# Optimization experiments

Hardware: AMD Instinct MI355X
Metric: run time of the kernel (lower is better)

## Reference

```python
import jax, jax.numpy as jnp
import numpy as np

NUM_HEADS = 16
KEY_DIM = 64
VALUE_DIM = 64
D_MODEL = 1024
NEG_INF = -1e10


def setup_inputs() -> dict:
    key = jax.random.key(0)
    ks = jax.random.split(key, 8)
    B, T, S, D = 4, 2048, 2048, D_MODEL
    w_scale = 1.0 / np.sqrt(D)  # keep logits well-scaled
    inp = {
        'query': jax.random.normal(ks[0], (B, T, D), jnp.float32),
        'key':   jax.random.normal(ks[1], (B, S, D), jnp.float32),
        'value': jax.random.normal(ks[2], (B, S, D), jnp.float32),
        'Wq': jax.random.normal(ks[3], (D, NUM_HEADS * KEY_DIM), jnp.float32) * w_scale,
        'bq': jnp.zeros((NUM_HEADS * KEY_DIM,), jnp.float32),
        'Wk': jax.random.normal(ks[4], (D, NUM_HEADS * KEY_DIM), jnp.float32) * w_scale,
        'bk': jnp.zeros((NUM_HEADS * KEY_DIM,), jnp.float32),
        'Wv': jax.random.normal(ks[5], (D, NUM_HEADS * VALUE_DIM), jnp.float32) * w_scale,
        'bv': jnp.zeros((NUM_HEADS * VALUE_DIM,), jnp.float32),
        'Wo': jax.random.normal(ks[6], (NUM_HEADS * VALUE_DIM, D), jnp.float32) * w_scale,
        'bo': jnp.zeros((D,), jnp.float32),
    }
    return inp


def reference(query, key, value, Wq, bq, Wk, bk, Wv, bv, Wo, bo):
    B, T, _ = query.shape
    S = key.shape[1]
    H, Dk, Dv = NUM_HEADS, KEY_DIM, VALUE_DIM
    # QKV projections -> (B, T/S, H, D_head)
    q = (query @ Wq + bq).reshape(B, T, H, Dk)
    k = (key @ Wk + bk).reshape(B, S, H, Dk)
    v = (value @ Wv + bv).reshape(B, S, H, Dv)
    # scaled dot-product scores: (B, H, T, S)
    q = q * (1.0 / jnp.sqrt(jnp.asarray(Dk, q.dtype)))
    scores = jnp.einsum('bthd,bshd->bhts', q, k)
    # causal mask [1,1,T,S], additive -1e10 on masked positions (as in source)
    causal = jnp.tril(jnp.ones((T, S), scores.dtype))
    scores = scores + NEG_INF * (1.0 - causal)
    attn = jax.nn.softmax(scores, axis=-1)
    # dropout rate = 0.0 -> identity
    ctx = jnp.einsum('bhts,bshd->bthd', attn, v).reshape(B, T, H * Dv)
    out = ctx @ Wo + bo
    return out
```

## Files before the change

kernel.cpp:

```cpp
#include <hip/hip_runtime.h>
#include <cstdint>

#define DEV static __device__ __forceinline__

typedef unsigned short u16;
typedef unsigned int u32;
using short8 = __attribute__((ext_vector_type(8))) short;
using f32x2  = __attribute__((ext_vector_type(2))) float;
using f32x4  = __attribute__((ext_vector_type(4))) float;
using f32x8  = __attribute__((ext_vector_type(8))) float;
using f32x16 = __attribute__((ext_vector_type(16))) float;
using u32x4  = __attribute__((ext_vector_type(4))) unsigned int;

constexpr int Bz = 4, Tz = 2048, Dz = 1024, Hz = 16;
constexpr float QSCALE = 0.125f * 1.4426950408889634f;

DEV u16 f2bf(float x) {
  union { float f; u32 u; } c; c.f = x;
  u32 u = c.u;
  return (u16)((u + 0x7FFFu + ((u >> 16) & 1u)) >> 16);
}

DEV u32 cvtpk(float a, float b) {
  u32 r;
  asm("v_cvt_pk_bf16_f32 %0, %1, %2" : "=v"(r) : "v"(a), "v"(b));
  return r;
}

DEV void gload16(const void* g, void* l) {
  __builtin_amdgcn_global_load_lds(
      (const __attribute__((address_space(1))) void*)g,
      (__attribute__((address_space(3))) void*)l, 16, 0, 0);
}

__global__ void wt_kernel(const float* __restrict__ W0, const float* __restrict__ W1,
                          const float* __restrict__ W2, const float* __restrict__ W3,
                          u16* __restrict__ T0, u16* __restrict__ T1,
                          u16* __restrict__ T2, u16* __restrict__ T3) {
  __shared__ float tile[32][33];
  int z = blockIdx.z;
  const float* W = z == 0 ? W0 : z == 1 ? W1 : z == 2 ? W2 : W3;
  u16* WT = z == 0 ? T0 : z == 1 ? T1 : z == 2 ? T2 : T3;
  int n0 = blockIdx.x * 32, k0 = blockIdx.y * 32;
  int tx = threadIdx.x & 31, ty = threadIdx.x >> 5;
  #pragma unroll
  for (int i = 0; i < 32; i += 8)
    tile[ty + i][tx] = W[(size_t)(k0 + ty + i) * Dz + n0 + tx];
  __syncthreads();
  #pragma unroll
  for (int i = 0; i < 32; i += 8)
    WT[(size_t)(n0 + ty + i) * Dz + k0 + tx] = f2bf(tile[tx][ty + i]);
}

template <int AFP32, int EPI>
DEV void gemm_core(const void* __restrict__ Aptr, const u16* __restrict__ WT,
                   const float* __restrict__ bias, void* __restrict__ Cptr,
                   float scale, int n0, int m0, char* L)
{
  constexpr int BOFF = AFP32 ? 32768 : 16384;

  const int tid = threadIdx.x;
  const int lane = tid & 63, wid = tid >> 6;
  const int g = lane >> 4, l15 = lane & 15;
  const int wm = (wid >> 1) * 64, wn = (wid & 1) * 64;

  f32x4 acc[4][4] = {};

  const int srow = tid >> 3, scolb = (tid & 7) * 16;
  const int scbs = scolb ^ ((srow & 7) << 4);
  const int frow = tid >> 4, fcolb = (tid & 15) * 16;
  const int fcbs = fcolb ^ ((frow & 7) << 4);

  for (int step = 0; step < 16; ++step) {
    const int k0 = step * 64;
    if (AFP32) {
      const float* A = (const float*)Aptr;
      #pragma unroll
      for (int i = 0; i < 8; ++i) {
        int row = frow + i * 16;
        gload16(A + (size_t)(m0 + row) * Dz + k0 + (fcbs >> 2),
                L + (tid + i * 256) * 16);
      }
    } else {
      const u16* A = (const u16*)Aptr;
      #pragma unroll
      for (int i = 0; i < 4; ++i) {
        int row = srow + i * 32;
        gload16(A + (size_t)(m0 + row) * Dz + k0 + (scbs >> 1),
                L + (tid + i * 256) * 16);
      }
    }
    #pragma unroll
    for (int i = 0; i < 4; ++i) {
      int row = srow + i * 32;
      gload16(WT + (size_t)(n0 + row) * Dz + k0 + (scbs >> 1),
              L + BOFF + (tid + i * 256) * 16);
    }
    __syncthreads();

    #pragma unroll
    for (int kc = 0; kc < 2; ++kc) {
      short8 af[4], bfv[4];
      #pragma unroll
      for (int mt = 0; mt < 4; ++mt) {
        int row = wm + mt * 16 + l15;
        if (AFP32) {
          int base = kc * 128 + g * 32;
          int sw = (row & 7) << 4;
          const char* pr = L + row * 256;
          f32x4 lo = *(const f32x4*)(pr + (base ^ sw));
          f32x4 hi = *(const f32x4*)(pr + ((base + 16) ^ sw));
          u32x4 w = {cvtpk(lo[0], lo[1]), cvtpk(lo[2], lo[3]),
                     cvtpk(hi[0], hi[1]), cvtpk(hi[2], hi[3])};
          af[mt] = __builtin_bit_cast(short8, w);
        } else {
          af[mt] = *(const short8*)(L + row * 128 + ((kc * 64 + g * 16) ^ ((row & 7) << 4)));
        }
      }
      #pragma unroll
      for (int nt = 0; nt < 4; ++nt) {
        int row = wn + nt * 16 + l15;
        bfv[nt] = *(const short8*)(L + BOFF + row * 128 + ((kc * 64 + g * 16) ^ ((row & 7) << 4)));
      }
      #pragma unroll
      for (int mt = 0; mt < 4; ++mt)
        #pragma unroll
        for (int nt = 0; nt < 4; ++nt)
          acc[mt][nt] = __builtin_amdgcn_mfma_f32_16x16x32_bf16(af[mt], bfv[nt], acc[mt][nt], 0, 0, 0);
    }
    __syncthreads();
  }

  if (EPI == 0) {
    u16* C = (u16*)Cptr;
    #pragma unroll
    for (int nt = 0; nt < 4; ++nt) {
      int n = n0 + wn + nt * 16 + l15;
      float bv = bias[n];
      #pragma unroll
      for (int mt = 0; mt < 4; ++mt)
        #pragma unroll
        for (int r = 0; r < 4; ++r) {
          int m = m0 + wm + mt * 16 + g * 4 + r;
          C[(size_t)m * Dz + n] = f2bf((acc[mt][nt][r] + bv) * scale);
        }
    }
  } else if (EPI == 1) {
    float* C = (float*)Cptr;
    #pragma unroll
    for (int nt = 0; nt < 4; ++nt) {
      int n = n0 + wn + nt * 16 + l15;
      float bv = bias[n];
      #pragma unroll
      for (int mt = 0; mt < 4; ++mt)
        #pragma unroll
        for (int r = 0; r < 4; ++r) {
          int m = m0 + wm + mt * 16 + g * 4 + r;
          C[(size_t)m * Dz + n] = acc[mt][nt][r] + bv;
        }
    }
  } else {
    u16* VT = (u16*)Cptr;
    #pragma unroll
    for (int nt = 0; nt < 4; ++nt) {
      int nrel = wn + nt * 16 + l15;
      float bv = bias[n0 + nrel];
      int swz = (nrel & 7) << 4;
      #pragma unroll
      for (int mt = 0; mt < 4; ++mt) {
        int mrel0 = wm + mt * 16 + g * 4;
        uint2 p = make_uint2(cvtpk(acc[mt][nt][0] + bv, acc[mt][nt][1] + bv),
                             cvtpk(acc[mt][nt][2] + bv, acc[mt][nt][3] + bv));
        *(uint2*)(L + nrel * 256 + ((mrel0 * 2) ^ swz)) = p;
      }
    }
    __syncthreads();
    int n = tid & 127, strip = tid >> 7;
    int nn = n0 + n;
    int h = nn >> 6, dv = nn & 63;
    int b = m0 >> 11;
    int tb = m0 & 2047;
    int swz = (n & 7) << 4;
    u16* dst = VT + (((size_t)(b * Hz + h) * 64 + dv) * Tz) + tb + strip * 64;
    #pragma unroll
    for (int c = 0; c < 8; ++c) {
      uint4 v = *(const uint4*)(L + n * 256 + ((strip * 128 + c * 16) ^ swz));
      *(uint4*)(dst + c * 8) = v;
    }
  }
}

__global__ __launch_bounds__(256, 3) void qkv_kernel(
    const float* __restrict__ Aq, const float* __restrict__ Ak, const float* __restrict__ Av,
    const u16* __restrict__ Wq, const u16* __restrict__ Wk, const u16* __restrict__ Wv,
    const float* __restrict__ bq, const float* __restrict__ bk, const float* __restrict__ bv,
    u16* __restrict__ oq, u16* __restrict__ ok, u16* __restrict__ ovt)
{
  __shared__ char lds[49152];
  int z = blockIdx.z;
  int n0 = blockIdx.y * 128, m0 = blockIdx.x * 128;
  if (z == 0)
    gemm_core<1, 0>(Aq, Wq, bq, oq, QSCALE, n0, m0, lds);
  else if (z == 1)
    gemm_core<1, 0>(Ak, Wk, bk, ok, 1.0f, n0, m0, lds);
  else
    gemm_core<1, 2>(Av, Wv, bv, ovt, 1.0f, n0, m0, lds);
}

__global__ __launch_bounds__(256, 4) void out_gemm_kernel(
    const u16* __restrict__ A, const u16* __restrict__ WT,
    const float* __restrict__ bias, float* __restrict__ C)
{
  __shared__ char lds[32768];
  gemm_core<0, 1>(A, WT, bias, C, 1.0f, blockIdx.y * 128, blockIdx.x * 128, lds);
}

DEV short8 mk_pb(float p0, float p1, float p2, float p3,
                 float p4, float p5, float p6, float p7) {
  u32 x0 = cvtpk(p0, p1), y0 = cvtpk(p4, p5);
  u32 x1 = cvtpk(p2, p3), y1 = cvtpk(p6, p7);
  asm("v_permlane32_swap_b32 %0, %1" : "+v"(x0), "+v"(y0));
  asm("v_permlane32_swap_b32 %0, %1" : "+v"(x1), "+v"(y1));
  u32x4 w = {x0, x1, y0, y1};
  return __builtin_bit_cast(short8, w);
}

DEV float vsum16(f32x16 a, f32x16 b) {
  f32x16 s = a + b;
  f32x8 s8 = __builtin_shufflevector(s, s, 0, 1, 2, 3, 4, 5, 6, 7) +
             __builtin_shufflevector(s, s, 8, 9, 10, 11, 12, 13, 14, 15);
  f32x4 s4 = __builtin_shufflevector(s8, s8, 0, 1, 2, 3) +
             __builtin_shufflevector(s8, s8, 4, 5, 6, 7);
  f32x2 s2 = __builtin_shufflevector(s4, s4, 0, 1) +
             __builtin_shufflevector(s4, s4, 2, 3);
  return s2[0] + s2[1];
}

__global__ __launch_bounds__(512) void attn_kernel(
    const u16* __restrict__ Q, const u16* __restrict__ K,
    const u16* __restrict__ VT, u16* __restrict__ CTX)
{
  __shared__ char lds[65536];

  const int tid = threadIdx.x;
  const int lane = tid & 63, wave = tid >> 6;
  const int s = wave >> 2, w4 = wave & 3;
  const int l31 = lane & 31, hi = lane >> 5;
  const int pr = blockIdx.y;
  const int bh = blockIdx.x;
  const int b = bh >> 4, h = bh & 15;

  const u16* qb  = Q  + (size_t)b * Tz * Dz + h * 64;
  const u16* kb  = K  + (size_t)b * Tz * Dz + h * 64;
  const u16* vtb = VT + (size_t)bh * 64 * Tz;

  #pragma unroll 1
  for (int half = 0; half < 2; ++half) {
    const int j = half ? (15 - pr) : pr;
    const int t0 = j * 128;
    const int nsteps = j + 1;
    const int wq0 = t0 + w4 * 32;
    const int qg = wq0 + l31, wqhi = wq0 + 31;
    const int tbase = s * nsteps;

    auto stage = [&](int buf, int step) {
      #pragma unroll
      for (int i = 0; i < 4; ++i) {
        int c = tid + i * 512;
        int sc = c >> 10, r = c & 1023;
        int tn = r >> 9, e = r & 511;
        int row = e >> 3, colb = (e & 7) * 16;
        int cbs = colb ^ ((row & 7) << 4);
        int kv0 = (sc * nsteps + step) * 64;
        char* dst = lds + ((sc * 2 + buf) << 14) + (tn << 13) + e * 16;
        if (tn == 0)
          gload16(kb + (size_t)(kv0 + row) * Dz + (cbs >> 1), dst);
        else
          gload16(vtb + (size_t)row * Tz + kv0 + (cbs >> 1), dst);
      }
    };

    stage(0, 0);

    short8 qf[4];
    #pragma unroll
    for (int kc = 0; kc < 4; ++kc)
      qf[kc] = *(const short8*)(qb + (size_t)qg * Dz + kc * 16 + hi * 8);

    f32x16 o0 = {}, o1 = {};
    float l_run = 0.f;

    __syncthreads();

    int cur = 0;
    for (int step = 0; step < nsteps; ++step) {
      if (step + 1 < nsteps) stage(cur ^ 1, step + 1);
      const int kv0 = (tbase + step) * 64;

      if (kv0 <= wqhi) {
        const char* Kl = lds + ((s * 2 + cur) << 14);
        const char* Vl = Kl + 8192;
        const int swz = (l31 & 7) << 4;

        f32x16 s0 = {}, s1 = {};
        __builtin_amdgcn_s_setprio(1);
        #pragma unroll
        for (int kc = 0; kc < 4; ++kc) {
          int cb = (kc * 32 + hi * 16) ^ swz;
          short8 kf0 = *(const short8*)(Kl + l31 * 128 + cb);
          short8 kf1 = *(const short8*)(Kl + (32 + l31) * 128 + cb);
          s0 = __builtin_amdgcn_mfma_f32_32x32x16_bf16(kf0, qf[kc], s0, 0, 0, 0);
          s1 = __builtin_amdgcn_mfma_f32_32x32x16_bf16(kf1, qf[kc], s1, 0, 0, 0);
        }
        __builtin_amdgcn_s_setprio(0);

        if (kv0 + 63 > wq0) {
          #pragma unroll
          for (int r = 0; r < 16; ++r) {
            int kg = kv0 + (r & 3) + 8 * (r >> 2) + 4 * hi;
            if (kg > qg)      s0[r] = -3.0e38f;
            if (kg + 32 > qg) s1[r] = -3.0e38f;
          }
        }

        #pragma unroll
        for (int r = 0; r < 16; ++r) {
          s0[r] = __builtin_amdgcn_exp2f(s0[r]);
          s1[r] = __builtin_amdgcn_exp2f(s1[r]);
        }
        float psum = vsum16(s0, s1);
        psum += __shfl_xor(psum, 32);
        l_run += psum;

        short8 pb0 = mk_pb(s0[0], s0[1], s0[2],  s0[3],  s0[4],  s0[5],  s0[6],  s0[7]);
        short8 pb1 = mk_pb(s0[8], s0[9], s0[10], s0[11], s0[12], s0[13], s0[14], s0[15]);
        short8 pb2 = mk_pb(s1[0], s1[1], s1[2],  s1[3],  s1[4],  s1[5],  s1[6],  s1[7]);
        short8 pb3 = mk_pb(s1[8], s1[9], s1[10], s1[11], s1[12], s1[13], s1[14], s1[15]);

        __builtin_amdgcn_s_setprio(1);
        #pragma unroll
        for (int kc = 0; kc < 4; ++kc) {
          int cb = (kc * 32 + hi * 16) ^ swz;
          short8 vf0 = *(const short8*)(Vl + l31 * 128 + cb);
          short8 vf1 = *(const short8*)(Vl + (32 + l31) * 128 + cb);
          short8 pbk = (kc == 0) ? pb0 : (kc == 1) ? pb1 : (kc == 2) ? pb2 : pb3;
          o0 = __builtin_amdgcn_mfma_f32_32x32x16_bf16(vf0, pbk, o0, 0, 0, 0);
          o1 = __builtin_amdgcn_mfma_f32_32x32x16_bf16(vf1, pbk, o1, 0, 0, 0);
        }
        __builtin_amdgcn_s_setprio(0);
      }

      __syncthreads();
      cur ^= 1;
    }

    if (s == 1) {
      char* P = lds + w4 * 9216 + lane * 144;
      #pragma unroll
      for (int r2 = 0; r2 < 4; ++r2) {
        f32x4 a = {o0[4*r2], o0[4*r2+1], o0[4*r2+2], o0[4*r2+3]};
        *(f32x4*)(P + r2 * 16) = a;
        f32x4 c = {o1[4*r2], o1[4*r2+1], o1[4*r2+2], o1[4*r2+3]};
        *(f32x4*)(P + 64 + r2 * 16) = c;
      }
      *(float*)(P + 128) = l_run;
    }
    __syncthreads();
    if (s == 0) {
      const char* P = lds + w4 * 9216 + lane * 144;
      float l1 = *(const float*)(P + 128);
      float inv = 1.0f / (l_run + l1);

      u16* cp = CTX + ((size_t)(b * Tz + qg)) * Dz + h * 64;
      #pragma unroll
      for (int rq = 0; rq < 4; ++rq) {
        f32x4 p0 = *(const f32x4*)(P + rq * 16);
        f32x4 p1 = *(const f32x4*)(P + 64 + rq * 16);
        int dv0 = 8 * rq + 4 * hi;
        float a0 = (o0[rq*4+0] + p0[0]) * inv;
        float a1 = (o0[rq*4+1] + p0[1]) * inv;
        float a2 = (o0[rq*4+2] + p0[2]) * inv;
        float a3 = (o0[rq*4+3] + p0[3]) * inv;
        *(uint2*)(cp + dv0) = make_uint2(cvtpk(a0, a1), cvtpk(a2, a3));
        float c0 = (o1[rq*4+0] + p1[0]) * inv;
        float c1 = (o1[rq*4+1] + p1[1]) * inv;
        float c2 = (o1[rq*4+2] + p1[2]) * inv;
        float c3 = (o1[rq*4+3] + p1[3]) * inv;
        *(uint2*)(cp + 32 + dv0) = make_uint2(cvtpk(c0, c1), cvtpk(c2, c3));
      }
    }
    __syncthreads();
  }
}

extern "C" void kernel_launch(void* const* d_in, const int* in_sizes, int n_in,
                              void* d_out, int out_size, void* d_ws, size_t ws_size,
                              hipStream_t stream) {
  (void)in_sizes; (void)n_in; (void)out_size; (void)ws_size;
  const float* query = (const float*)d_in[0];
  const float* key   = (const float*)d_in[1];
  const float* value = (const float*)d_in[2];
  const float* Wq = (const float*)d_in[3];
  const float* bq = (const float*)d_in[4];
  const float* Wk = (const float*)d_in[5];
  const float* bk = (const float*)d_in[6];
  const float* Wv = (const float*)d_in[7];
  const float* bv = (const float*)d_in[8];
  const float* Wo = (const float*)d_in[9];
  const float* bo = (const float*)d_in[10];

  char* ws = (char*)d_ws;
  const size_t SZ_ACT = (size_t)Bz * Tz * Dz * sizeof(u16);
  const size_t SZ_W = (size_t)Dz * Dz * sizeof(u16);
  u16* qw  = (u16*)(ws);
  u16* kw  = (u16*)(ws + SZ_ACT);
  u16* cw  = (u16*)(ws + 2 * SZ_ACT);
  u16* vtw = (u16*)(ws + 3 * SZ_ACT);
  u16* wqt = (u16*)(ws + 4 * SZ_ACT);
  u16* wkt = (u16*)(ws + 4 * SZ_ACT + SZ_W);
  u16* wvt = (u16*)(ws + 4 * SZ_ACT + 2 * SZ_W);
  u16* wot = (u16*)(ws + 4 * SZ_ACT + 3 * SZ_W);

  wt_kernel<<<dim3(32, 32, 4), 256, 0, stream>>>(Wq, Wk, Wv, Wo, wqt, wkt, wvt, wot);

  qkv_kernel<<<dim3(64, 8, 3), 256, 0, stream>>>(query, key, value,
                                                 wqt, wkt, wvt,
                                                 bq, bk, bv,
                                                 qw, kw, vtw);

  attn_kernel<<<dim3(Bz * Hz, 8), 512, 0, stream>>>(qw, kw, vtw, cw);

  out_gemm_kernel<<<dim3(64, 8), 256, 0, stream>>>(cw, wot, bo, (float*)d_out);
}
```

Measured before the change: 163.7 us.

## Halve fp32 A-tile K-depth in QKV GEMM to cut LDS and raise occupancy

The fp32-input QKV GEMM now stages A in 32-wide K slices (16 KB) instead of 64-wide (32 KB), loading the bf16 weight tile every other step. This drops the kernel's LDS from 48 KB to 32 KB and raises launch bounds from 3 to 5 blocks per CU to increase occupancy. In exchange it doubles the number of barrier-separated steps, halving MFMA work per sync. An extra barrier is added before the V-transpose epilogue, which reuses LDS.

```diff
diff --git a/kernel.cpp b/kernel.cpp
--- a/kernel.cpp
+++ b/kernel.cpp
@@ -57,8 +57,6 @@
                    const float* __restrict__ bias, void* __restrict__ Cptr,
                    float scale, int n0, int m0, char* L)
 {
-  constexpr int BOFF = AFP32 ? 32768 : 16384;
-
   const int tid = threadIdx.x;
   const int lane = tid & 63, wid = tid >> 6;
   const int g = lane >> 4, l15 = lane & 15;
@@ -68,67 +66,94 @@
 
   const int srow = tid >> 3, scolb = (tid & 7) * 16;
   const int scbs = scolb ^ ((srow & 7) << 4);
-  const int frow = tid >> 4, fcolb = (tid & 15) * 16;
-  const int fcbs = fcolb ^ ((frow & 7) << 4);
-
-  for (int step = 0; step < 16; ++step) {
-    const int k0 = step * 64;
-    if (AFP32) {
-      const float* A = (const float*)Aptr;
-      #pragma unroll
-      for (int i = 0; i < 8; ++i) {
-        int row = frow + i * 16;
-        gload16(A + (size_t)(m0 + row) * Dz + k0 + (fcbs >> 2),
-                L + (tid + i * 256) * 16);
-      }
-    } else {
-      const u16* A = (const u16*)Aptr;
+
+  if (AFP32) {
+    const float* A = (const float*)Aptr;
+    for (int step = 0; step < 32; ++step) {
+      const int k0f = step * 32;
+      #pragma unroll
+      for (int i = 0; i < 4; ++i) {
+        int c = tid + i * 256;
+        int row = c >> 3;
+        gload16(A + (size_t)(m0 + row) * Dz + k0f + (scbs >> 2),
+                L + c * 16);
+      }
+      if ((step & 1) == 0) {
+        int k0 = (step >> 1) * 64;
+        #pragma unroll
+        for (int i = 0; i < 4; ++i) {
+          int c = tid + i * 256;
+          int row = c >> 3;
+          gload16(WT + (size_t)(n0 + row) * Dz + k0 + (scbs >> 1),
+                  L + 16384 + c * 16);
+        }
+      }
+      __syncthreads();
+
+      const int kc = step & 1;
+      short8 af[4], bfv[4];
+      #pragma unroll
+      for (int mt = 0; mt < 4; ++mt) {
+        int row = wm + mt * 16 + l15;
+        int sw = (row & 7) << 4;
+        const char* pr = L + row * 128;
+        f32x4 lo = *(const f32x4*)(pr + ((g * 32) ^ sw));
+        f32x4 hi = *(const f32x4*)(pr + ((g * 32 + 16) ^ sw));
+        u32x4 w = {cvtpk(lo[0], lo[1]), cvtpk(lo[2], lo[3]),
+                   cvtpk(hi[0], hi[1]), cvtpk(hi[2], hi[3])};
+        af[mt] = __builtin_bit_cast(short8, w);
+      }
+      #pragma unroll
+      for (int nt = 0; nt < 4; ++nt) {
+        int row = wn + nt * 16 + l15;
+        bfv[nt] = *(const short8*)(L + 16384 + row * 128 + ((kc * 64 + g * 16) ^ ((row & 7) << 4)));
+      }
+      #pragma unroll
+      for (int mt = 0; mt < 4; ++mt)
+        #pragma unroll
+        for (int nt = 0; nt < 4; ++nt)
+          acc[mt][nt] = __builtin_amdgcn_mfma_f32_16x16x32_bf16(af[mt], bfv[nt], acc[mt][nt], 0, 0, 0);
+      __syncthreads();
+    }
+  } else {
+    const u16* A = (const u16*)Aptr;
+    for (int step = 0; step < 16; ++step) {
+      const int k0 = step * 64;
       #pragma unroll
       for (int i = 0; i < 4; ++i) {
         int row = srow + i * 32;
         gload16(A + (size_t)(m0 + row) * Dz + k0 + (scbs >> 1),
                 L + (tid + i * 256) * 16);
       }
-    }
-    #pragma unroll
-    for (int i = 0; i < 4; ++i) {
-      int row = srow + i * 32;
-      gload16(WT + (size_t)(n0 + row) * Dz + k0 + (scbs >> 1),
-              L + BOFF + (tid + i * 256) * 16);
-    }
-    __syncthreads();
-
-    #pragma unroll
-    for (int kc = 0; kc < 2; ++kc) {
-      short8 af[4], bfv[4];
-      #pragma unroll
-      for (int mt = 0; mt < 4; ++mt) {
-        int row = wm + mt * 16 + l15;
-        if (AFP32) {
-          int base = kc * 128 + g * 32;
-          int sw = (row & 7) << 4;
-          const char* pr = L + row * 256;
-          f32x4 lo = *(const f32x4*)(pr + (base ^ sw));
-          f32x4 hi = *(const f32x4*)(pr + ((base + 16) ^ sw));
-          u32x4 w = {cvtpk(lo[0], lo[1]), cvtpk(lo[2], lo[3]),
-                     cvtpk(hi[0], hi[1]), cvtpk(hi[2], hi[3])};
-          af[mt] = __builtin_bit_cast(short8, w);
-        } else {
+      #pragma unroll
+      for (int i = 0; i < 4; ++i) {
+        int row = srow + i * 32;
+        gload16(WT + (size_t)(n0 + row) * Dz + k0 + (scbs >> 1),
+                L + 16384 + (tid + i * 256) * 16);
+      }
+      __syncthreads();
+
+      #pragma unroll
+      for (int kc = 0; kc < 2; ++kc) {
+        short8 af[4], bfv[4];
+        #pragma unroll
+        for (int mt = 0; mt < 4; ++mt) {
+          int row = wm + mt * 16 + l15;
           af[mt] = *(const short8*)(L + row * 128 + ((kc * 64 + g * 16) ^ ((row & 7) << 4)));
         }
-      }
-      #pragma unroll
-      for (int nt = 0; nt < 4; ++nt) {
-        int row = wn + nt * 16 + l15;
-        bfv[nt] = *(const short8*)(L + BOFF + row * 128 + ((kc * 64 + g * 16) ^ ((row & 7) << 4)));
-      }
-      #pragma unroll
-      for (int mt = 0; mt < 4; ++mt)
-        #pragma unroll
-        for (int nt = 0; nt < 4; ++nt)
-          acc[mt][nt] = __builtin_amdgcn_mfma_f32_16x16x32_bf16(af[mt], bfv[nt], acc[mt][nt], 0, 0, 0);
-    }
-    __syncthreads();
+        #pragma unroll
+        for (int nt = 0; nt < 4; ++nt) {
+          int row = wn + nt * 16 + l15;
+          bfv[nt] = *(const short8*)(L + 16384 + row * 128 + ((kc * 64 + g * 16) ^ ((row & 7) << 4)));
+        }
+        #pragma unroll
+        for (int mt = 0; mt < 4; ++mt)
+          #pragma unroll
+          for (int nt = 0; nt < 4; ++nt)
+            acc[mt][nt] = __builtin_amdgcn_mfma_f32_16x16x32_bf16(af[mt], bfv[nt], acc[mt][nt], 0, 0, 0);
+      }
+      __syncthreads();
+    }
   }
 
   if (EPI == 0) {
@@ -161,6 +186,7 @@
     }
   } else {
     u16* VT = (u16*)Cptr;
+    __syncthreads();
     #pragma unroll
     for (int nt = 0; nt < 4; ++nt) {
       int nrel = wn + nt * 16 + l15;
@@ -190,13 +216,13 @@
   }
 }
 
-__global__ __launch_bounds__(256, 3) void qkv_kernel(
+__global__ __launch_bounds__(256, 5) void qkv_kernel(
     const float* __restrict__ Aq, const float* __restrict__ Ak, const float* __restrict__ Av,
     const u16* __restrict__ Wq, const u16* __restrict__ Wk, const u16* __restrict__ Wv,
     const float* __restrict__ bq, const float* __restrict__ bk, const float* __restrict__ bv,
     u16* __restrict__ oq, u16* __restrict__ ok, u16* __restrict__ ovt)
 {
-  __shared__ char lds[49152];
+  __shared__ char lds[32768];
   int z = blockIdx.z;
   int n0 = blockIdx.y * 128, m0 = blockIdx.x * 128;
   if (z == 0)
```

Measured after the change: 476.5 us. 191% more time.
